# Optimization experiments

Hardware: AMD Instinct MI355X
Metric: run time of the kernel (lower is better)

Reference implementation:

```python
import jax, jax.numpy as jnp
import numpy as np

N = 1536       # number of agents in the group
T = 20         # track length (only last step used)
H = 64         # hidden_size
E = 16         # embadding_size
M = 128        # PNMLP_hidden_size


def setup_inputs() -> dict:
    key = jax.random.key(0)
    ks = jax.random.split(key, 8)
    s = lambda fan_in: 1.0 / np.sqrt(fan_in)
    return {
        "hidden_state": jax.random.normal(ks[0], (N, H), dtype=jnp.float32),
        "group_track": jax.random.normal(ks[1], (N, T, 2), dtype=jnp.float32),
        "We": jax.random.uniform(ks[2], (2, E), jnp.float32, -s(2), s(2)),
        "be": jax.random.uniform(ks[3], (E,), jnp.float32, -s(2), s(2)),
        "W1": jax.random.uniform(ks[4], (E + H, M), jnp.float32, -s(E + H), s(E + H)),
        "b1": jax.random.uniform(ks[5], (M,), jnp.float32, -s(E + H), s(E + H)),
        "W2": jax.random.uniform(ks[6], (M, H), jnp.float32, -s(M), s(M)),
        "b2": jax.random.uniform(ks[7], (H,), jnp.float32, -s(M), s(M)),
    }


def reference(hidden_state, group_track, We, be, W1, b1, W2, b2):
    # end positions of every track: [N, 2]
    end = group_track[:, -1, :]
    # rel[i, j] = end[j] - end[i]  (neighbor j relative to center i): [N, N, 2]
    rel = end[None, :, :] - end[:, None, :]
    # linear embedding of relative end positions: [N, N, E]
    emb = rel @ We + be
    # concat hidden state (same for all centers) with embedding: [N, N, E+H]
    h = jnp.broadcast_to(hidden_state[None, :, :], (rel.shape[0], rel.shape[1], hidden_state.shape[1]))
    x = jnp.concatenate((h, emb), axis=-1)
    # MLP [E+H -> M -> H] with ReLU after each linear (batch_norm=False)
    x = jax.nn.relu(x @ W1 + b1)
    x = jax.nn.relu(x @ W2 + b2)
    # max-pool over neighbors j for each center i: [N, H]
    return jnp.max(x, axis=1)
```

## Files before the change

kernel.cpp:

```cpp
#include <hip/hip_runtime.h>


#define NN 1536
#define HH 64
#define EE 16
#define MM 128
#define TT 20

#define WAVES 4
#define IBLK  WAVES
#define NIBLK (NN / IBLK)
#define JSPLIT 2
#define NTILE (96 / JSPLIT)
#define TILEB 4096

typedef _Float16 half8 __attribute__((ext_vector_type(8)));
typedef float f32x4 __attribute__((ext_vector_type(4)));

__device__ __forceinline__ void gload_lds16(const void* g, void* l) {
  auto gp = (const __attribute__((address_space(1))) unsigned int*)g;
  auto lp = (__attribute__((address_space(3))) unsigned int*)l;
  __builtin_amdgcn_global_load_lds(gp, lp, 16, 0, 0);
}

__global__ __launch_bounds__(128) void precompute_kernel(
    const float* __restrict__ hidden, const float* __restrict__ gt,
    const float* __restrict__ We, const float* __restrict__ be,
    const float* __restrict__ W1, const float* __restrict__ b1,
    _Float16* __restrict__ Qf, _Float16* __restrict__ P, float* __restrict__ out)
{
  const int j = blockIdx.x;
  const int m = threadIdx.x;
  const float* hrow = hidden + j * HH;
  float a0 = 0.f, a1 = 0.f;
  #pragma unroll 8
  for (int h = 0; h < HH; h += 2) {
    a0 = fmaf(hrow[h],     W1[h * MM + m],       a0);
    a1 = fmaf(hrow[h + 1], W1[(h + 1) * MM + m], a1);
  }
  const float a = a0 + a1;
  float ve0 = 0.f, ve1 = 0.f, cm = b1[m];
  #pragma unroll
  for (int e = 0; e < EE; ++e) {
    float w1e = W1[(HH + e) * MM + m];
    ve0 = fmaf(We[e], w1e, ve0);
    ve1 = fmaf(We[EE + e], w1e, ve1);
    cm  = fmaf(be[e], w1e, cm);
  }
  const float e0 = gt[j * (2 * TT) + 2 * (TT - 1)];
  const float e1 = gt[j * (2 * TT) + 2 * (TT - 1) + 1];
  const float p = fmaf(e0, ve0, e1 * ve1);
  P[j * MM + m] = (_Float16)p;

  const int jt = j >> 4;
  const int ks = m >> 5;
  const int ln = ((m >> 3) & 3) * 16 + (j & 15);
  const int jj = m & 7;
  Qf[(((jt * 4) + ks) * 64 + ln) * 8 + jj] = (_Float16)(a + p + cm);

  if (m < HH) out[j * HH + m] = 0.f;
}

__global__ __launch_bounds__(256, 3) void pairmlp_max_kernel(
    const _Float16* __restrict__ Qf, const _Float16* __restrict__ P,
    const float* __restrict__ W2, const float* __restrict__ b2,
    float* __restrict__ out)
{
  __shared__ half8 qlds[2 * 256];

  const int tid  = threadIdx.x;
  const int wid  = tid >> 6;
  const int lane = tid & 63;
  const int quad = lane >> 4;
  const int lcol = lane & 15;
  const int ig = blockIdx.x % NIBLK;
  const int js = blockIdx.x / NIBLK;
  const int i  = ig * IBLK + wid;

  half8 bfrag[4][4];
  #pragma unroll
  for (int ct = 0; ct < 4; ++ct) {
    #pragma unroll
    for (int ks = 0; ks < 4; ++ks) {
      half8 b;
      #pragma unroll
      for (int jj = 0; jj < 8; ++jj)
        b[jj] = (_Float16)W2[(ks * 32 + quad * 8 + jj) * HH + ct * 16 + lcol];
      bfrag[ct][ks] = b;
    }
  }

  half8 pv[4];
  #pragma unroll
  for (int ks = 0; ks < 4; ++ks)
    pv[ks] = *(const half8*)(P + i * MM + ks * 32 + quad * 8);

  float rmax[4];
  #pragma unroll
  for (int ct = 0; ct < 4; ++ct) rmax[ct] = -3.0e38f;

  const int jt0 = js * NTILE;
  const char* qsrc = (const char*)Qf + (size_t)jt0 * TILEB + wid * 1024 + lane * 16;
  char* qdst = (char*)qlds + wid * 1024;

  const half8 hz = 0;

  gload_lds16(qsrc, qdst);
  __syncthreads();

  int buf = 0;
  for (int t = 0; t < NTILE; ++t) {
    if (t + 1 < NTILE)
      gload_lds16(qsrc + (size_t)(t + 1) * TILEB, qdst + (buf ^ 1) * TILEB);

    const half8* ql = qlds + buf * 256;
    f32x4 acc[4];

    {
      half8 s = ql[lane] - pv[0];
      s = __builtin_elementwise_max(s, hz);
      #pragma unroll
      for (int ct = 0; ct < 4; ++ct)
        acc[ct] = __builtin_amdgcn_mfma_f32_16x16x32_f16(s, bfrag[ct][0], f32x4{0.f, 0.f, 0.f, 0.f}, 0, 0, 0);
    }
    #pragma unroll
    for (int ks = 1; ks < 4; ++ks) {
      half8 s = ql[ks * 64 + lane] - pv[ks];
      s = __builtin_elementwise_max(s, hz);
      #pragma unroll
      for (int ct = 0; ct < 4; ++ct)
        acc[ct] = __builtin_amdgcn_mfma_f32_16x16x32_f16(s, bfrag[ct][ks], acc[ct], 0, 0, 0);
    }

    #pragma unroll
    for (int ct = 0; ct < 4; ++ct) {
      const float m01 = fmaxf(acc[ct][0], acc[ct][1]);
      const float m23 = fmaxf(acc[ct][2], acc[ct][3]);
      rmax[ct] = fmaxf(rmax[ct], fmaxf(m01, m23));
    }

    __syncthreads();
    buf ^= 1;
  }

  #pragma unroll
  for (int ct = 0; ct < 4; ++ct) {
    float v = rmax[ct];
    v = fmaxf(v, __shfl_xor(v, 16, 64));
    v = fmaxf(v, __shfl_xor(v, 32, 64));
    v = fmaxf(v + b2[ct * 16 + lcol], 0.f);
    if (quad == 0)
      atomicMax((unsigned*)(out + i * HH + ct * 16 + lcol), __float_as_uint(v));
  }
}

extern "C" void kernel_launch(void* const* d_in, const int* in_sizes, int n_in,
                              void* d_out, int out_size, void* d_ws, size_t ws_size,
                              hipStream_t stream) {
  const float* hidden = (const float*)d_in[0];
  const float* gt     = (const float*)d_in[1];
  const float* We     = (const float*)d_in[2];
  const float* be     = (const float*)d_in[3];
  const float* W1     = (const float*)d_in[4];
  const float* b1     = (const float*)d_in[5];
  const float* W2     = (const float*)d_in[6];
  const float* b2     = (const float*)d_in[7];
  float* out = (float*)d_out;

  _Float16* Qf = (_Float16*)d_ws;
  _Float16* Ph = Qf + NN * MM;

  precompute_kernel<<<NN, 128, 0, stream>>>(hidden, gt, We, be, W1, b1, Qf, Ph, out);
  pairmlp_max_kernel<<<NIBLK * JSPLIT, 256, 0, stream>>>(Qf, Ph, W2, b2, out);
}
```

Before: 115.7 us.

## Use single-wave blocks with register-prefetched Q tiles instead of shared LDS staging

The pair-MLP kernel now runs one wave per block, one center per block. It loads Q tiles straight from global memory into registers with a one-tile-ahead prefetch, replacing the shared LDS double buffer and its block barriers. W2 is converted to fp16 MFMA fragment layout once in the precompute kernel, so each block does coalesced half8 loads instead of strided float gathers. Each wave still reads every Q tile, now through L2 rather than from an LDS tile shared by four waves. That raises cache traffic in exchange for dropping synchronisation.

```diff
diff --git a/kernel.cpp b/kernel.cpp
--- a/kernel.cpp
+++ b/kernel.cpp
@@ -7,27 +7,19 @@
 #define MM 128
 #define TT 20
 
-#define WAVES 4
-#define IBLK  WAVES
-#define NIBLK (NN / IBLK)
 #define JSPLIT 2
 #define NTILE (96 / JSPLIT)
-#define TILEB 4096
 
 typedef _Float16 half8 __attribute__((ext_vector_type(8)));
 typedef float f32x4 __attribute__((ext_vector_type(4)));
-
-__device__ __forceinline__ void gload_lds16(const void* g, void* l) {
-  auto gp = (const __attribute__((address_space(1))) unsigned int*)g;
-  auto lp = (__attribute__((address_space(3))) unsigned int*)l;
-  __builtin_amdgcn_global_load_lds(gp, lp, 16, 0, 0);
-}
 
 __global__ __launch_bounds__(128) void precompute_kernel(
     const float* __restrict__ hidden, const float* __restrict__ gt,
     const float* __restrict__ We, const float* __restrict__ be,
     const float* __restrict__ W1, const float* __restrict__ b1,
-    _Float16* __restrict__ Qf, _Float16* __restrict__ P, float* __restrict__ out)
+    const float* __restrict__ W2,
+    _Float16* __restrict__ Qf, _Float16* __restrict__ P,
+    _Float16* __restrict__ W2f, float* __restrict__ out)
 {
   const int j = blockIdx.x;
   const int m = threadIdx.x;
@@ -59,35 +51,39 @@
   Qf[(((jt * 4) + ks) * 64 + ln) * 8 + jj] = (_Float16)(a + p + cm);
 
   if (m < HH) out[j * HH + m] = 0.f;
+
+  if (j < 8) {
+    const int u = j * 128 + m;
+    const int ct = u >> 8;
+    const int ksx = (u >> 6) & 3;
+    const int l = u & 63;
+    half8 w;
+    #pragma unroll
+    for (int t = 0; t < 8; ++t)
+      w[t] = (_Float16)W2[(ksx * 32 + (l >> 4) * 8 + t) * HH + ct * 16 + (l & 15)];
+    *(half8*)(W2f + (size_t)u * 8) = w;
+  }
 }
 
-__global__ __launch_bounds__(256, 3) void pairmlp_max_kernel(
+__global__ __launch_bounds__(64, 3) void pairmlp_max_kernel(
     const _Float16* __restrict__ Qf, const _Float16* __restrict__ P,
-    const float* __restrict__ W2, const float* __restrict__ b2,
+    const _Float16* __restrict__ W2f, const float* __restrict__ b2,
     float* __restrict__ out)
 {
-  __shared__ half8 qlds[2 * 256];
-
-  const int tid  = threadIdx.x;
-  const int wid  = tid >> 6;
-  const int lane = tid & 63;
+  const int lane = threadIdx.x;
   const int quad = lane >> 4;
   const int lcol = lane & 15;
-  const int ig = blockIdx.x % NIBLK;
-  const int js = blockIdx.x / NIBLK;
-  const int i  = ig * IBLK + wid;
+  const int i  = blockIdx.x % NN;
+  const int js = blockIdx.x / NN;
 
   half8 bfrag[4][4];
-  #pragma unroll
-  for (int ct = 0; ct < 4; ++ct) {
+  {
+    const half8* wf = (const half8*)W2f + lane;
     #pragma unroll
-    for (int ks = 0; ks < 4; ++ks) {
-      half8 b;
+    for (int ct = 0; ct < 4; ++ct)
       #pragma unroll
-      for (int jj = 0; jj < 8; ++jj)
-        b[jj] = (_Float16)W2[(ks * 32 + quad * 8 + jj) * HH + ct * 16 + lcol];
-      bfrag[ct][ks] = b;
-    }
+      for (int ks = 0; ks < 4; ++ks)
+        bfrag[ct][ks] = wf[(ct * 4 + ks) * 64];
   }
 
   half8 pv[4];
@@ -95,29 +91,32 @@
   for (int ks = 0; ks < 4; ++ks)
     pv[ks] = *(const half8*)(P + i * MM + ks * 32 + quad * 8);
 
+  float b2v[4];
+  #pragma unroll
+  for (int ct = 0; ct < 4; ++ct) b2v[ct] = b2[ct * 16 + lcol];
+
   float rmax[4];
   #pragma unroll
   for (int ct = 0; ct < 4; ++ct) rmax[ct] = -3.0e38f;
 
   const int jt0 = js * NTILE;
-  const char* qsrc = (const char*)Qf + (size_t)jt0 * TILEB + wid * 1024 + lane * 16;
-  char* qdst = (char*)qlds + wid * 1024;
+  const half8* qbase = (const half8*)Qf + (size_t)jt0 * 256 + lane;
+
+  half8 qc[4], qn[4];
+  #pragma unroll
+  for (int ks = 0; ks < 4; ++ks) qc[ks] = qbase[ks * 64];
 
   const half8 hz = 0;
 
-  gload_lds16(qsrc, qdst);
-  __syncthreads();
+  for (int t = 0; t < NTILE; ++t) {
+    const int tn = (t + 1 < NTILE) ? (t + 1) : 0;
+    #pragma unroll
+    for (int ks = 0; ks < 4; ++ks)
+      qn[ks] = qbase[(size_t)tn * 256 + ks * 64];
 
-  int buf = 0;
-  for (int t = 0; t < NTILE; ++t) {
-    if (t + 1 < NTILE)
-      gload_lds16(qsrc + (size_t)(t + 1) * TILEB, qdst + (buf ^ 1) * TILEB);
-
-    const half8* ql = qlds + buf * 256;
     f32x4 acc[4];
-
     {
-      half8 s = ql[lane] - pv[0];
+      half8 s = qc[0] - pv[0];
       s = __builtin_elementwise_max(s, hz);
       #pragma unroll
       for (int ct = 0; ct < 4; ++ct)
@@ -125,7 +124,7 @@
     }
     #pragma unroll
     for (int ks = 1; ks < 4; ++ks) {
-      half8 s = ql[ks * 64 + lane] - pv[ks];
+      half8 s = qc[ks] - pv[ks];
       s = __builtin_elementwise_max(s, hz);
       #pragma unroll
       for (int ct = 0; ct < 4; ++ct)
@@ -139,8 +138,8 @@
       rmax[ct] = fmaxf(rmax[ct], fmaxf(m01, m23));
     }
 
-    __syncthreads();
-    buf ^= 1;
+    #pragma unroll
+    for (int ks = 0; ks < 4; ++ks) qc[ks] = qn[ks];
   }
 
   #pragma unroll
@@ -148,7 +147,7 @@
     float v = rmax[ct];
     v = fmaxf(v, __shfl_xor(v, 16, 64));
     v = fmaxf(v, __shfl_xor(v, 32, 64));
-    v = fmaxf(v + b2[ct * 16 + lcol], 0.f);
+    v = fmaxf(v + b2v[ct], 0.f);
     if (quad == 0)
       atomicMax((unsigned*)(out + i * HH + ct * 16 + lcol), __float_as_uint(v));
   }
@@ -167,9 +166,10 @@
   const float* b2     = (const float*)d_in[7];
   float* out = (float*)d_out;
 
-  _Float16* Qf = (_Float16*)d_ws;
-  _Float16* Ph = Qf + NN * MM;
+  _Float16* Qf  = (_Float16*)d_ws;
+  _Float16* Ph  = Qf + NN * MM;
+  _Float16* W2f = Ph + NN * MM;
 
-  precompute_kernel<<<NN, 128, 0, stream>>>(hidden, gt, We, be, W1, b1, Qf, Ph, out);
-  pairmlp_max_kernel<<<NIBLK * JSPLIT, 256, 0, stream>>>(Qf, Ph, W2, b2, out);
+  precompute_kernel<<<NN, 128, 0, stream>>>(hidden, gt, We, be, W1, b1, W2, Qf, Ph, W2f, out);
+  pairmlp_max_kernel<<<NN * JSPLIT, 64, 0, stream>>>(Qf, Ph, W2f, b2, out);
 }
```

After: 119.4 us. 1.03x slower.
